# Kernel tuning notes

Hardware: AMD Instinct MI355X
Metric: run time of the kernel (lower is better)

Reference implementation:

```python
import jax, jax.numpy as jnp
import numpy as np

B, S, D = 2, 2048, 1024
KQ_EMB, V_EMB, H = 1024, 1024, 16
KQ_HD, V_HD = KQ_EMB // H, V_EMB // H


def setup_inputs() -> dict:
    key = jax.random.key(0)
    ks = jax.random.split(key, 7)
    scale = 1.0 / np.sqrt(D)
    return {
        "q": jax.random.normal(ks[0], (B, S, D), dtype=jnp.float32),
        "k": jax.random.normal(ks[1], (B, S, D), dtype=jnp.float32),
        "v": jax.random.normal(ks[2], (B, S, D), dtype=jnp.float32),
        "Wq": jax.random.normal(ks[3], (D, KQ_EMB), dtype=jnp.float32) * scale,
        "Wk": jax.random.normal(ks[4], (D, KQ_EMB), dtype=jnp.float32) * scale,
        "Wv": jax.random.normal(ks[5], (D, V_EMB), dtype=jnp.float32) * scale,
        "Wo": jax.random.normal(ks[6], (V_EMB, V_EMB), dtype=jnp.float32) * (1.0 / np.sqrt(V_EMB)),
        "masked": 1,
    }


def reference(q, k, v, Wq, Wk, Wv, Wo, masked):
    Bq, Sq, _ = q.shape
    # projections (Linear, no bias)
    Q = (q @ Wq).reshape(Bq, Sq, H, KQ_HD).transpose(0, 2, 1, 3)  # [B,H,S,hd]
    K = (k @ Wk).reshape(Bq, Sq, H, KQ_HD).transpose(0, 2, 1, 3)
    V = (v @ Wv).reshape(Bq, Sq, H, V_HD).transpose(0, 2, 1, 3)
    scores = jnp.einsum("bhqd,bhkd->bhqk", Q, K) * (1.0 / KQ_HD ** 0.5)
    if masked:
        causal = jnp.tril(jnp.ones((Sq, Sq), dtype=bool))  # True = keep
        scores = jnp.where(causal, scores, jnp.float32(-jnp.inf))
    weights = jax.nn.softmax(scores, axis=-1)
    attn_out = jnp.einsum("bhqk,bhkd->bhqd", weights, V)  # [B,H,S,v_hd]
    merged = attn_out.transpose(0, 2, 1, 3).reshape(Bq, Sq, H * V_HD)
    output = merged @ Wo
    return output, attn_out
```

## Files before the change

### kernel.cpp

```cpp
#include <hip/hip_runtime.h>
#include <math.h>

constexpr int CB = 2, CS = 2048, CD = 1024, CH = 16, CHD = 64;
constexpr int CEMB = 1024;

typedef unsigned short ushort_t;
typedef __attribute__((ext_vector_type(8))) short short8;
typedef __attribute__((ext_vector_type(4))) float f32x4;

__device__ __forceinline__ ushort_t f2bf(float x) {
    unsigned int u = __builtin_bit_cast(unsigned int, x);
    u = u + 0x7fffu + ((u >> 16) & 1u);
    return (ushort_t)(u >> 16);
}
__device__ __forceinline__ float bf2f(ushort_t h) {
    unsigned int u = ((unsigned int)h) << 16;
    return __builtin_bit_cast(float, u);
}

__global__ __launch_bounds__(256) void convert_wt(
    const float* __restrict__ W0, const float* __restrict__ W1,
    const float* __restrict__ W2, const float* __restrict__ W3,
    ushort_t* __restrict__ H0, ushort_t* __restrict__ L0,
    ushort_t* __restrict__ H1, ushort_t* __restrict__ L1,
    ushort_t* __restrict__ H2, ushort_t* __restrict__ L2,
    ushort_t* __restrict__ H3, ushort_t* __restrict__ L3) {
    const float* W;
    ushort_t* Hd;
    ushort_t* Ld;
    switch (blockIdx.z) {
        case 0: W = W0; Hd = H0; Ld = L0; break;
        case 1: W = W1; Hd = H1; Ld = L1; break;
        case 2: W = W2; Hd = H2; Ld = L2; break;
        default: W = W3; Hd = H3; Ld = L3; break;
    }
    const int n0 = blockIdx.x * 64, k0 = blockIdx.y * 64;
    __shared__ float Ls[64][65];
    const int t = threadIdx.x;
#pragma unroll
    for (int rep = 0; rep < 4; rep++) {
        const int r = rep * 16 + (t >> 4);
        const int c4 = (t & 15) * 4;
        *(float4*)&Ls[r][c4] = *(const float4*)&W[(size_t)(k0 + r) * CEMB + n0 + c4];
    }
    __syncthreads();
    const int n = t >> 2, kc = (t & 3) * 16;
#pragma unroll
    for (int c = 0; c < 2; c++) {
        union { ushort_t us[8]; uint4 v; } H, L;
#pragma unroll
        for (int j = 0; j < 8; j++) {
            const float x = Ls[kc + c * 8 + j][n];
            const ushort_t h = f2bf(x);
            H.us[j] = h;
            L.us[j] = f2bf(x - bf2f(h));
        }
        const size_t dst = (size_t)(n0 + n) * CEMB + k0 + kc + c * 8;
        *(uint4*)&Hd[dst] = H.v;
        *(uint4*)&Ld[dst] = L.v;
    }
}

constexpr int LP = 72;

template <bool GATHER_A>
__device__ __forceinline__ void gemm_split_body(
    const float* __restrict__ A, const ushort_t* __restrict__ Bhi,
    const ushort_t* __restrict__ Blo, float* __restrict__ Cf,
    ushort_t* __restrict__ C0, ushort_t* __restrict__ C1, float scale,
    int emode, int M, int N, int K) {
    __shared__ char gpool[36864];
    ushort_t* const As_hi = (ushort_t*)gpool;
    ushort_t* const As_lo = As_hi + 128 * 32;
    ushort_t* const Bs_hi = As_lo + 128 * 32;
    ushort_t* const Bs_lo = Bs_hi + 128 * 32;
    const int tid = threadIdx.x;
    const int row0 = blockIdx.y * 128, col0 = blockIdx.x * 128;
    const int w = tid >> 6, l = tid & 63, lr = l & 15, lg = l >> 4;
    const int wm = w >> 1, wn = w & 1;

    f32x4 acc[4][4];
#pragma unroll
    for (int i = 0; i < 4; i++)
#pragma unroll
        for (int j = 0; j < 4; j++) acc[i][j] = (f32x4)(0.f);

    const int st_r = tid >> 1;
    const int st_kh = (tid & 1) * 16;

    for (int k0 = 0; k0 < K; k0 += 32) {
        {
            const int gm = row0 + st_r;
            const int gk = k0 + st_kh;
            const float* src;
            if (GATHER_A) {
                const int b_ = gm >> 11, s_ = gm & 2047;
                const int h_ = gk >> 6, d_ = gk & 63;
                src = &A[(((size_t)b_ * CH + h_) * CS + s_) * CHD + d_];
            } else {
                src = &A[(size_t)gm * K + gk];
            }
            float va[16];
#pragma unroll
            for (int r = 0; r < 4; r++)
                *(float4*)&va[r * 4] = *(const float4*)&src[r * 4];
#pragma unroll
            for (int c = 0; c < 2; c++) {
                union { ushort_t us[8]; uint4 v; } H, L;
#pragma unroll
                for (int j = 0; j < 8; j++) {
                    const float x = va[c * 8 + j];
                    const ushort_t h = f2bf(x);
                    H.us[j] = h;
                    L.us[j] = f2bf(x - bf2f(h));
                }
                const int chunk = (st_kh >> 3) + c;
                const int csw = chunk ^ ((st_r >> 1) & 3);
                *(uint4*)&As_hi[st_r * 32 + csw * 8] = H.v;
                *(uint4*)&As_lo[st_r * 32 + csw * 8] = L.v;
            }
        }
        {
            const size_t base = (size_t)(col0 + st_r) * K + k0 + st_kh;
#pragma unroll
            for (int c = 0; c < 2; c++) {
                const uint4 hv = *(const uint4*)&Bhi[base + c * 8];
                const uint4 lv = *(const uint4*)&Blo[base + c * 8];
                const int chunk = (st_kh >> 3) + c;
                const int csw = chunk ^ ((st_r >> 1) & 3);
                *(uint4*)&Bs_hi[st_r * 32 + csw * 8] = hv;
                *(uint4*)&Bs_lo[st_r * 32 + csw * 8] = lv;
            }
        }
        __syncthreads();

        short8 ah[4], al[4], bh[4], bl[4];
#pragma unroll
        for (int i = 0; i < 4; i++) {
            const int r = wm * 64 + i * 16 + lr;
            const int cs = lg ^ ((r >> 1) & 3);
            ah[i] = *(const short8*)&As_hi[r * 32 + cs * 8];
            al[i] = *(const short8*)&As_lo[r * 32 + cs * 8];
        }
#pragma unroll
        for (int j = 0; j < 4; j++) {
            const int cc = wn * 64 + j * 16 + lr;
            const int cs = lg ^ ((cc >> 1) & 3);
            bh[j] = *(const short8*)&Bs_hi[cc * 32 + cs * 8];
            bl[j] = *(const short8*)&Bs_lo[cc * 32 + cs * 8];
        }
#pragma unroll
        for (int j = 0; j < 4; j++)
#pragma unroll
            for (int i = 0; i < 4; i++) {
                acc[i][j] = __builtin_amdgcn_mfma_f32_16x16x32_bf16(
                    al[i], bh[j], acc[i][j], 0, 0, 0);
                acc[i][j] = __builtin_amdgcn_mfma_f32_16x16x32_bf16(
                    ah[i], bl[j], acc[i][j], 0, 0, 0);
                acc[i][j] = __builtin_amdgcn_mfma_f32_16x16x32_bf16(
                    ah[i], bh[j], acc[i][j], 0, 0, 0);
            }
        __syncthreads();
    }

    if (emode == 2) {
        ushort_t* const T = (ushort_t*)gpool + w * 64 * LP;
#pragma unroll
        for (int i = 0; i < 4; i++)
#pragma unroll
            for (int j = 0; j < 4; j++) {
                const unsigned int a =
                    (unsigned int)f2bf(acc[i][j][0]) |
                    ((unsigned int)f2bf(acc[i][j][1]) << 16);
                const unsigned int b =
                    (unsigned int)f2bf(acc[i][j][2]) |
                    ((unsigned int)f2bf(acc[i][j][3]) << 16);
                *(uint2*)&T[(j * 16 + lr) * LP + i * 16 + 4 * lg] =
                    make_uint2(a, b);
            }
#pragma unroll
        for (int grp = 0; grp < 8; grp++) {
            const int dl = (l >> 3) + grp * 8;
            const int s8 = (l & 7) * 8;
            const uint4 vv = *(const uint4*)&T[dl * LP + s8];
            const int gm = row0 + wm * 64 + s8;
            const int b_ = gm >> 11, ss = gm & 2047;
            const int dg = col0 + wn * 64 + dl;
            const int h_ = dg >> 6, hd = dg & 63;
            *(uint4*)&C0[(((size_t)b_ * CH + h_) * CHD + hd) * CS + ss] = vv;
        }
        return;
    }

#pragma unroll
    for (int i = 0; i < 4; i++)
#pragma unroll
        for (int j = 0; j < 4; j++) {
            const int cc = col0 + wn * 64 + j * 16 + lr;
#pragma unroll
            for (int r = 0; r < 4; r++) {
                const int cr = row0 + wm * 64 + i * 16 + lg * 4 + r;
                const float vv = acc[i][j][r];
                if (emode == 0) {
                    Cf[(size_t)cr * N + cc] = vv;
                } else {
                    const int b_ = cr >> 11, s_ = cr & 2047;
                    const int h_ = cc >> 6, d_ = cc & 63;
                    const size_t idx =
                        (((size_t)b_ * CH + h_) * CS + s_) * CHD + d_;
                    const float x = vv * scale;
                    const ushort_t hb = f2bf(x);
                    C0[idx] = hb;
                    C1[idx] = f2bf(x - bf2f(hb));
                }
            }
        }
}

__global__ __launch_bounds__(256, 2) void qkv_proj(
    const float* __restrict__ q, const float* __restrict__ k,
    const float* __restrict__ v,
    const ushort_t* __restrict__ hq, const ushort_t* __restrict__ lq,
    const ushort_t* __restrict__ hk, const ushort_t* __restrict__ lk,
    const ushort_t* __restrict__ hv, const ushort_t* __restrict__ lv,
    ushort_t* __restrict__ Qhi, ushort_t* __restrict__ Qlo,
    ushort_t* __restrict__ Khi, ushort_t* __restrict__ Klo,
    ushort_t* __restrict__ Vt) {
    const float* A;
    const ushort_t* Bh;
    const ushort_t* Bl;
    ushort_t* C0;
    ushort_t* C1 = nullptr;
    float scale = 1.0f;
    int emode;
    if (blockIdx.z == 0) {
        A = q; Bh = hq; Bl = lq; C0 = Qhi; C1 = Qlo; scale = 0.125f; emode = 1;
    } else if (blockIdx.z == 1) {
        A = k; Bh = hk; Bl = lk; C0 = Khi; C1 = Klo; emode = 1;
    } else {
        A = v; Bh = hv; Bl = lv; C0 = Vt; emode = 2;
    }
    gemm_split_body<false>(A, Bh, Bl, nullptr, C0, C1, scale, emode,
                           CB * CS, CEMB, CD);
}

__global__ __launch_bounds__(256, 2) void out_proj(
    const float* __restrict__ attn, const ushort_t* __restrict__ ho,
    const ushort_t* __restrict__ lo_, float* __restrict__ out) {
    gemm_split_body<true>(attn, ho, lo_, out, nullptr, nullptr, 1.0f, 0,
                          CB * CS, CEMB, CEMB);
}

constexpr int PB = 136;
constexpr int PF = 68;

__global__ __launch_bounds__(256, 2) void flash_mfma(
    const ushort_t* __restrict__ Qhi, const ushort_t* __restrict__ Qlo,
    const ushort_t* __restrict__ Khi, const ushort_t* __restrict__ Klo,
    const ushort_t* __restrict__ Vt, float* __restrict__ O,
    const int* __restrict__ maskedp) {
    __shared__ ushort_t lds[3 * 64 * LP + 4 * 16 * PB];
    ushort_t* const Ks_hi = lds;
    ushort_t* const Ks_lo = lds + 64 * LP;
    ushort_t* const Vs = lds + 2 * 64 * LP;

    const int tid = threadIdx.x;
    const int w = tid >> 6, l = tid & 63, lr = l & 15, lg = l >> 4;
    ushort_t* const Ps = lds + 3 * 64 * LP + w * 16 * PB;
    float* const T = (float*)Ps;
    const int masked = maskedp[0];

    const int id = blockIdx.x + 16 * blockIdx.y;
    const int sid = (id & 7) * 64 + (id >> 3);
    const int jj = sid & 15;
    const int bh = sid >> 4;
    const int qa = 31 - jj;
    const size_t bhoff = (size_t)bh * CS * CHD;

    const int itersA = masked ? (32 - jj) : 32;
    const int TOT = itersA + (masked ? (jj + 1) : 32);

    short8 qh[2], ql[2];
    auto loadQ = [&](int qt) {
        const int q0 = qt * 64 + w * 16;
#pragma unroll
        for (int ds = 0; ds < 2; ds++) {
            const size_t off =
                bhoff + (size_t)(q0 + lr) * CHD + ds * 32 + lg * 8;
            qh[ds] = *(const short8*)&Qhi[off];
            ql[ds] = *(const short8*)&Qlo[off];
        }
    };

    f32x4 Oacc[4];
    float m_i, l_i;
    auto resetState = [&]() {
        m_i = -INFINITY;
        l_i = 0.f;
#pragma unroll
        for (int df = 0; df < 4; df++) Oacc[df] = (f32x4)(0.f);
    };

    auto writeO = [&](int qt) {
        const int q0 = qt * 64 + w * 16;
        const float inv = 1.0f / l_i;
#pragma unroll
        for (int df = 0; df < 4; df++)
            *(f32x4*)&T[lr * PF + df * 16 + 4 * lg] = Oacc[df] * inv;
#pragma unroll
        for (int grp = 0; grp < 4; grp++) {
            const int qrow = grp * 4 + lg;
            const float4 vv = *(const float4*)&T[qrow * PF + lr * 4];
            *(float4*)&O[bhoff + (size_t)(q0 + qrow) * CHD + lr * 4] = vv;
        }
    };

    loadQ(qa);
    resetState();

    const int st_r = tid >> 2;
    const int st_c = tid & 3;

    uint4 pk_hi[2], pk_lo[2], pv[2];
#pragma unroll
    for (int p = 0; p < 2; p++) {
        const int c = st_c + p * 4;
        const size_t kgl = bhoff + (size_t)st_r * CHD + c * 8;
        pk_hi[p] = *(const uint4*)&Khi[kgl];
        pk_lo[p] = *(const uint4*)&Klo[kgl];
        const size_t vgl = ((size_t)bh * CHD + st_r) * CS + c * 8;
        pv[p] = *(const uint4*)&Vt[vgl];
    }

    for (int it = 0; it < TOT; it++) {
        const bool inB = it >= itersA;
        const int t = inB ? (it - itersA) : it;
        const int qtcur = inB ? jj : qa;

#pragma unroll
        for (int p = 0; p < 2; p++) {
            const int c = st_c + p * 4;
            *(uint4*)&Ks_hi[st_r * LP + c * 8] = pk_hi[p];
            *(uint4*)&Ks_lo[st_r * LP + c * 8] = pk_lo[p];
            *(uint4*)&Vs[st_r * LP + c * 8] = pv[p];
        }
        __syncthreads();

        const int nit = it + 1;
        if (nit < TOT) {
            const int nt = (nit >= itersA) ? (nit - itersA) : nit;
#pragma unroll
            for (int p = 0; p < 2; p++) {
                const int c = st_c + p * 4;
                const size_t kgl =
                    bhoff + (size_t)(nt * 64 + st_r) * CHD + c * 8;
                pk_hi[p] = *(const uint4*)&Khi[kgl];
                pk_lo[p] = *(const uint4*)&Klo[kgl];
                const size_t vgl =
                    ((size_t)bh * CHD + st_r) * CS + nt * 64 + c * 8;
                pv[p] = *(const uint4*)&Vt[vgl];
            }
        }

        f32x4 S[4];
#pragma unroll
        for (int kf = 0; kf < 4; kf++) S[kf] = (f32x4)(0.f);
#pragma unroll
        for (int ds = 0; ds < 2; ds++) {
            short8 kh[4], kl[4];
#pragma unroll
            for (int kf = 0; kf < 4; kf++) {
                const int off = (kf * 16 + lr) * LP + ds * 32 + lg * 8;
                kh[kf] = *(const short8*)&Ks_hi[off];
                kl[kf] = *(const short8*)&Ks_lo[off];
            }
#pragma unroll
            for (int kf = 0; kf < 4; kf++) {
                S[kf] = __builtin_amdgcn_mfma_f32_16x16x32_bf16(
                    kh[kf], ql[ds], S[kf], 0, 0, 0);
                S[kf] = __builtin_amdgcn_mfma_f32_16x16x32_bf16(
                    kl[kf], qh[ds], S[kf], 0, 0, 0);
                S[kf] = __builtin_amdgcn_mfma_f32_16x16x32_bf16(
                    kh[kf], qh[ds], S[kf], 0, 0, 0);
            }
        }

        if (masked && t == qtcur) {
            const int qg = qtcur * 64 + w * 16 + lr;
#pragma unroll
            for (int kf = 0; kf < 4; kf++)
#pragma unroll
                for (int r = 0; r < 4; r++) {
                    const int kg = t * 64 + kf * 16 + 4 * lg + r;
                    if (kg > qg) S[kf][r] = -INFINITY;
                }
        }

        {
            float mt = -INFINITY;
#pragma unroll
            for (int kf = 0; kf < 4; kf++)
#pragma unroll
                for (int r = 0; r < 4; r++) mt = fmaxf(mt, S[kf][r]);
            mt = fmaxf(mt, __shfl_xor(mt, 16));
            mt = fmaxf(mt, __shfl_xor(mt, 32));
            const float mn = fmaxf(m_i, mt);
            const float corr = __expf(m_i - mn);
            float rs = 0.f;
#pragma unroll
            for (int kf = 0; kf < 4; kf++)
#pragma unroll
                for (int r = 0; r < 4; r++) {
                    const float p = __expf(S[kf][r] - mn);
                    S[kf][r] = p;
                    rs += p;
                }
            rs += __shfl_xor(rs, 16);
            rs += __shfl_xor(rs, 32);
            l_i = l_i * corr + rs;
            m_i = mn;
#pragma unroll
            for (int df = 0; df < 4; df++) Oacc[df] *= corr;
        }

#pragma unroll
        for (int kf = 0; kf < 4; kf++) {
            const unsigned int a = (unsigned int)f2bf(S[kf][0]) |
                                   ((unsigned int)f2bf(S[kf][1]) << 16);
            const unsigned int b = (unsigned int)f2bf(S[kf][2]) |
                                   ((unsigned int)f2bf(S[kf][3]) << 16);
            *(uint2*)&Ps[lr * PB + kf * 16 + 4 * lg] = make_uint2(a, b);
        }

#pragma unroll
        for (int ks = 0; ks < 2; ks++) {
            short8 vb[4];
#pragma unroll
            for (int df = 0; df < 4; df++)
                vb[df] = *(const short8*)&Vs[(df * 16 + lr) * LP + ks * 32 +
                                             lg * 8];
            const short8 pb = *(const short8*)&Ps[lr * PB + ks * 32 + lg * 8];
#pragma unroll
            for (int df = 0; df < 4; df++)
                Oacc[df] = __builtin_amdgcn_mfma_f32_16x16x32_bf16(
                    vb[df], pb, Oacc[df], 0, 0, 0);
        }

        if (it == itersA - 1) {
            writeO(qa);
            resetState();
            loadQ(jj);
        }
        __syncthreads();
    }

    writeO(jj);
}

extern "C" void kernel_launch(void* const* d_in, const int* in_sizes, int n_in,
                              void* d_out, int out_size, void* d_ws,
                              size_t ws_size, hipStream_t stream) {
    const float* q  = (const float*)d_in[0];
    const float* k  = (const float*)d_in[1];
    const float* v  = (const float*)d_in[2];
    const float* Wq = (const float*)d_in[3];
    const float* Wk = (const float*)d_in[4];
    const float* Wv = (const float*)d_in[5];
    const float* Wo = (const float*)d_in[6];
    const int* masked = (const int*)d_in[7];

    float* out  = (float*)d_out;
    float* attn = out + (size_t)CB * CS * CEMB;

    const size_t NE = (size_t)CB * CS * CEMB;
    ushort_t* wsb = (ushort_t*)d_ws;
    ushort_t* Qhi = wsb + 0 * NE;
    ushort_t* Qlo = wsb + 1 * NE;
    ushort_t* Khi = wsb + 2 * NE;
    ushort_t* Klo = wsb + 3 * NE;
    ushort_t* Vt  = wsb + 4 * NE;
    ushort_t* wb  = wsb + 5 * NE;
    const size_t WN = (size_t)CEMB * CEMB;
    ushort_t* hq = wb + 0 * WN;  ushort_t* lq = wb + 1 * WN;
    ushort_t* hk = wb + 2 * WN;  ushort_t* lk = wb + 3 * WN;
    ushort_t* hv = wb + 4 * WN;  ushort_t* lv = wb + 5 * WN;
    ushort_t* ho = wb + 6 * WN;  ushort_t* lo_ = wb + 7 * WN;

    const int M = CB * CS;
    dim3 blk(256);

    convert_wt<<<dim3(16, 16, 4), blk, 0, stream>>>(
        Wq, Wk, Wv, Wo, hq, lq, hk, lk, hv, lv, ho, lo_);

    qkv_proj<<<dim3(CEMB / 128, M / 128, 3), blk, 0, stream>>>(
        q, k, v, hq, lq, hk, lk, hv, lv, Qhi, Qlo, Khi, Klo, Vt);

    flash_mfma<<<dim3(16, CB * CH), blk, 0, stream>>>(
        Qhi, Qlo, Khi, Klo, Vt, attn, masked);

    out_proj<<<dim3(CEMB / 128, M / 128), blk, 0, stream>>>(attn, ho, lo_, out);
}
```

Before: 357.0 us.

## Drop split-bf16 correction terms for V projection, remap GEMM blocks, add MFMA priority

The V projection now runs only the hi*hi bf16 MFMA and skips loading, storing and multiplying the low-part correction terms, because its output is rounded to single bf16 anyway. The QKV and output GEMMs are launched on a 1D grid whose block order runs down rows within a column tile, which should improve L2 reuse of the weight tiles. The flash kernel raises wave priority around its MFMA sections. Dropping the correction terms for V lowers its precision toward plain bf16, which may affect accuracy.

```diff
diff --git a/kernel.cpp b/kernel.cpp
--- a/kernel.cpp
+++ b/kernel.cpp
@@ -68,14 +68,13 @@
     const float* __restrict__ A, const ushort_t* __restrict__ Bhi,
     const ushort_t* __restrict__ Blo, float* __restrict__ Cf,
     ushort_t* __restrict__ C0, ushort_t* __restrict__ C1, float scale,
-    int emode, int M, int N, int K) {
+    int emode, bool full, int row0, int col0, int M, int N, int K) {
     __shared__ char gpool[36864];
     ushort_t* const As_hi = (ushort_t*)gpool;
     ushort_t* const As_lo = As_hi + 128 * 32;
     ushort_t* const Bs_hi = As_lo + 128 * 32;
     ushort_t* const Bs_lo = Bs_hi + 128 * 32;
     const int tid = threadIdx.x;
-    const int row0 = blockIdx.y * 128, col0 = blockIdx.x * 128;
     const int w = tid >> 6, l = tid & 63, lr = l & 15, lg = l >> 4;
     const int wm = w >> 1, wn = w & 1;
 
@@ -117,19 +116,20 @@
                 const int chunk = (st_kh >> 3) + c;
                 const int csw = chunk ^ ((st_r >> 1) & 3);
                 *(uint4*)&As_hi[st_r * 32 + csw * 8] = H.v;
-                *(uint4*)&As_lo[st_r * 32 + csw * 8] = L.v;
+                if (full) *(uint4*)&As_lo[st_r * 32 + csw * 8] = L.v;
             }
         }
         {
             const size_t base = (size_t)(col0 + st_r) * K + k0 + st_kh;
 #pragma unroll
             for (int c = 0; c < 2; c++) {
-                const uint4 hv = *(const uint4*)&Bhi[base + c * 8];
-                const uint4 lv = *(const uint4*)&Blo[base + c * 8];
                 const int chunk = (st_kh >> 3) + c;
                 const int csw = chunk ^ ((st_r >> 1) & 3);
-                *(uint4*)&Bs_hi[st_r * 32 + csw * 8] = hv;
-                *(uint4*)&Bs_lo[st_r * 32 + csw * 8] = lv;
+                *(uint4*)&Bs_hi[st_r * 32 + csw * 8] =
+                    *(const uint4*)&Bhi[base + c * 8];
+                if (full)
+                    *(uint4*)&Bs_lo[st_r * 32 + csw * 8] =
+                        *(const uint4*)&Blo[base + c * 8];
             }
         }
         __syncthreads();
@@ -140,23 +140,25 @@
             const int r = wm * 64 + i * 16 + lr;
             const int cs = lg ^ ((r >> 1) & 3);
             ah[i] = *(const short8*)&As_hi[r * 32 + cs * 8];
-            al[i] = *(const short8*)&As_lo[r * 32 + cs * 8];
+            if (full) al[i] = *(const short8*)&As_lo[r * 32 + cs * 8];
         }
 #pragma unroll
         for (int j = 0; j < 4; j++) {
             const int cc = wn * 64 + j * 16 + lr;
             const int cs = lg ^ ((cc >> 1) & 3);
             bh[j] = *(const short8*)&Bs_hi[cc * 32 + cs * 8];
-            bl[j] = *(const short8*)&Bs_lo[cc * 32 + cs * 8];
+            if (full) bl[j] = *(const short8*)&Bs_lo[cc * 32 + cs * 8];
         }
 #pragma unroll
         for (int j = 0; j < 4; j++)
 #pragma unroll
             for (int i = 0; i < 4; i++) {
-                acc[i][j] = __builtin_amdgcn_mfma_f32_16x16x32_bf16(
-                    al[i], bh[j], acc[i][j], 0, 0, 0);
-                acc[i][j] = __builtin_amdgcn_mfma_f32_16x16x32_bf16(
-                    ah[i], bl[j], acc[i][j], 0, 0, 0);
+                if (full) {
+                    acc[i][j] = __builtin_amdgcn_mfma_f32_16x16x32_bf16(
+                        al[i], bh[j], acc[i][j], 0, 0, 0);
+                    acc[i][j] = __builtin_amdgcn_mfma_f32_16x16x32_bf16(
+                        ah[i], bl[j], acc[i][j], 0, 0, 0);
+                }
                 acc[i][j] = __builtin_amdgcn_mfma_f32_16x16x32_bf16(
                     ah[i], bh[j], acc[i][j], 0, 0, 0);
             }
@@ -226,6 +228,11 @@
     ushort_t* __restrict__ Qhi, ushort_t* __restrict__ Qlo,
     ushort_t* __restrict__ Khi, ushort_t* __restrict__ Klo,
     ushort_t* __restrict__ Vt) {
+    const int id = blockIdx.x;
+    const int col = id / 96;
+    const int rem = id % 96;
+    const int z = rem >> 5;
+    const int row = rem & 31;
     const float* A;
     const ushort_t* Bh;
     const ushort_t* Bl;
@@ -233,22 +240,26 @@
     ushort_t* C1 = nullptr;
     float scale = 1.0f;
     int emode;
-    if (blockIdx.z == 0) {
+    bool full = true;
+    if (z == 0) {
         A = q; Bh = hq; Bl = lq; C0 = Qhi; C1 = Qlo; scale = 0.125f; emode = 1;
-    } else if (blockIdx.z == 1) {
+    } else if (z == 1) {
         A = k; Bh = hk; Bl = lk; C0 = Khi; C1 = Klo; emode = 1;
     } else {
-        A = v; Bh = hv; Bl = lv; C0 = Vt; emode = 2;
-    }
-    gemm_split_body<false>(A, Bh, Bl, nullptr, C0, C1, scale, emode,
-                           CB * CS, CEMB, CD);
+        A = v; Bh = hv; Bl = lv; C0 = Vt; emode = 2; full = false;
+    }
+    gemm_split_body<false>(A, Bh, Bl, nullptr, C0, C1, scale, emode, full,
+                           row * 128, col * 128, CB * CS, CEMB, CD);
 }
 
 __global__ __launch_bounds__(256, 2) void out_proj(
     const float* __restrict__ attn, const ushort_t* __restrict__ ho,
     const ushort_t* __restrict__ lo_, float* __restrict__ out) {
-    gemm_split_body<true>(attn, ho, lo_, out, nullptr, nullptr, 1.0f, 0,
-                          CB * CS, CEMB, CEMB);
+    const int id = blockIdx.x;
+    const int col = id >> 5;
+    const int row = id & 31;
+    gemm_split_body<true>(attn, ho, lo_, out, nullptr, nullptr, 1.0f, 0, true,
+                          row * 128, col * 128, CB * CS, CEMB, CEMB);
 }
 
 constexpr int PB = 136;
@@ -365,6 +376,7 @@
         f32x4 S[4];
 #pragma unroll
         for (int kf = 0; kf < 4; kf++) S[kf] = (f32x4)(0.f);
+        __builtin_amdgcn_s_setprio(1);
 #pragma unroll
         for (int ds = 0; ds < 2; ds++) {
             short8 kh[4], kl[4];
@@ -384,6 +396,7 @@
                     kh[kf], qh[ds], S[kf], 0, 0, 0);
             }
         }
+        __builtin_amdgcn_s_setprio(0);
 
         if (masked && t == qtcur) {
             const int qg = qtcur * 64 + w * 16 + lr;
@@ -432,6 +445,7 @@
             *(uint2*)&Ps[lr * PB + kf * 16 + 4 * lg] = make_uint2(a, b);
         }
 
+        __builtin_amdgcn_s_setprio(1);
 #pragma unroll
         for (int ks = 0; ks < 2; ks++) {
             short8 vb[4];
@@ -445,6 +459,7 @@
                 Oacc[df] = __builtin_amdgcn_mfma_f32_16x16x32_bf16(
                     vb[df], pb, Oacc[df], 0, 0, 0);
         }
+        __builtin_amdgcn_s_setprio(0);
 
         if (it == itersA - 1) {
             writeO(qa);
@@ -486,17 +501,16 @@
     ushort_t* hv = wb + 4 * WN;  ushort_t* lv = wb + 5 * WN;
     ushort_t* ho = wb + 6 * WN;  ushort_t* lo_ = wb + 7 * WN;
 
-    const int M = CB * CS;
     dim3 blk(256);
 
     convert_wt<<<dim3(16, 16, 4), blk, 0, stream>>>(
         Wq, Wk, Wv, Wo, hq, lq, hk, lk, hv, lv, ho, lo_);
 
-    qkv_proj<<<dim3(CEMB / 128, M / 128, 3), blk, 0, stream>>>(
+    qkv_proj<<<dim3(768), blk, 0, stream>>>(
         q, k, v, hq, lq, hk, lk, hv, lv, Qhi, Qlo, Khi, Klo, Vt);
 
     flash_mfma<<<dim3(16, CB * CH), blk, 0, stream>>>(
         Qhi, Qlo, Khi, Klo, Vt, attn, masked);
 
-    out_proj<<<dim3(CEMB / 128, M / 128), blk, 0, stream>>>(attn, ho, lo_, out);
-}
+    out_proj<<<dim3(256), blk, 0, stream>>>(attn, ho, lo_, out);
+}
```

Measured after the change: 349.3 us. 1.02x faster.
